# Kernel tuning notes

Hardware: AMD Instinct MI355X
Metric: run time of the kernel (lower is better)

The kernel has to match this reference:

```python
import jax, jax.numpy as jnp
import numpy as np

UNITS = 512
M = 8
INPUT_DIM = 512
BATCH = 2048


def setup_inputs() -> dict:
    key = jax.random.key(0)
    ks = jax.random.split(key, 9)
    D, U = INPUT_DIM, UNITS
    fused_dim = D + U
    def glorot(k, shape):
        lim = np.sqrt(6.0 / (shape[0] + shape[1])).astype(np.float32)
        return jax.random.uniform(k, shape, jnp.float32, -lim, lim)
    return {
        "inputs": jax.random.normal(ks[0], (BATCH, D), jnp.float32),
        "elapsed": jax.random.uniform(ks[1], (BATCH, 1), jnp.float32),
        "state": jax.random.normal(ks[2], (BATCH, U * M), jnp.float32),
        "W_r": glorot(ks[3], (fused_dim, U * M)),
        "b_r": jnp.zeros((U * M,), jnp.float32),
        "W_d": glorot(ks[4], (fused_dim, U)),
        "b_d": jnp.zeros((U,), jnp.float32),
        "W_u": glorot(ks[5], (fused_dim, U * M)),
        "b_u": jnp.zeros((U * M,), jnp.float32),
    }


def reference(inputs, elapsed, state, W_r, b_r, W_d, b_d, W_u, b_u):
    B = inputs.shape[0]
    # tau_i = 10**(i/2)  =>  ln_tau_i = i * 0.5 * ln(10)
    ln_tau_table = 0.5 * jnp.log(jnp.float32(10.0)) * jnp.arange(M, dtype=jnp.float32)  # [M]
    tau_table = jnp.exp(ln_tau_table)  # [M]

    h_hat = state.reshape(B, UNITS, M)            # [B, U, M]
    h = h_hat.sum(axis=2)                          # [B, U]
    fused = jnp.concatenate([inputs, h], axis=-1)  # [B, D+U]

    # retrieval gate: softmax over M buckets of -(ln_tau_r - table)^2
    ln_tau_r = (fused @ W_r + b_r).reshape(B, UNITS, M)
    rki = jax.nn.softmax(-jnp.square(ln_tau_r - ln_tau_table), axis=2)
    q_input = jnp.sum(rki * h_hat, axis=2)         # [B, U]

    # detect (candidate) with tanh
    reset_value = jnp.concatenate([inputs, q_input], axis=1)
    qk = jnp.tanh(reset_value @ W_d + b_d)[:, :, None]  # [B, U, 1]

    # update gate
    ln_tau_s = (fused @ W_u + b_u).reshape(B, UNITS, M)
    ski = jax.nn.softmax(-jnp.square(ln_tau_s - ln_tau_table), axis=2)

    # exponential decay per bucket: elapsed [B,1] / tau [M] -> [B, M]
    exp_term = jnp.exp(-elapsed / tau_table)[:, None, :]  # [B, 1, M]
    h_hat_next = ((1.0 - ski) * h_hat + ski * qk) * exp_term  # [B, U, M]

    h_next = h_hat_next.sum(axis=2)                # [B, U]
    return h_next, h_hat_next.reshape(B, UNITS * M)
```

## Files before the change

kernel.cpp:

```cpp
#include <hip/hip_runtime.h>
#include <hip/hip_fp16.h>
#include <cmath>

#define B_SZ 2048
#define D_IN 512
#define U_N  512
#define FD   1024
#define NRU  4096
#define NRU2 8192

typedef _Float16 f16x8 __attribute__((ext_vector_type(8)));
typedef float    f32x4 __attribute__((ext_vector_type(4)));

typedef const __attribute__((address_space(1))) void glb_cv;
typedef __attribute__((address_space(3))) void lds_v;

#define TAB_INIT {0.0f, 1.15129254649702f, 2.30258509299405f, \
                  3.45387763949107f, 4.60517018598809f, 5.75646273248511f, \
                  6.90775527898214f, 8.05904782547916f}

__global__ __launch_bounds__(256) void prep_kernel(
    const float* __restrict__ inputs, const float* __restrict__ state,
    __half* __restrict__ fused, __half* __restrict__ reset)
{
    const int b = blockIdx.x;
    const int t = threadIdx.x;

    const float2 iv = *(const float2*)(inputs + (size_t)b * D_IN + t * 2);
    __half2 hv;
    hv.x = __float2half(iv.x);
    hv.y = __float2half(iv.y);
    *(__half2*)(fused + (size_t)b * FD + t * 2) = hv;
    *(__half2*)(reset + (size_t)b * FD + t * 2) = hv;

    const float4* sp = (const float4*)(state + (size_t)b * NRU + t * 16);
    float4 x0 = sp[0], x1 = sp[1], x2 = sp[2], x3 = sp[3];
    float s0 = (x0.x + x0.y) + (x0.z + x0.w) + (x1.x + x1.y) + (x1.z + x1.w);
    float s1 = (x2.x + x2.y) + (x2.z + x2.w) + (x3.x + x3.y) + (x3.z + x3.w);
    __half2 h2;
    h2.x = __float2half(s0);
    h2.y = __float2half(s1);
    *(__half2*)(fused + (size_t)b * FD + D_IN + t * 2) = h2;
}

__global__ __launch_bounds__(256) void convT3_kernel(
    const float* __restrict__ W_r, const float* __restrict__ W_u,
    const float* __restrict__ W_d, __half* __restrict__ WruT,
    __half* __restrict__ WdT)
{
    __shared__ float tile[32][33];
    const int bx = blockIdx.x;
    const float* W;
    __half* Wt;
    int N, nt;
    if (bx < 128)      { W = W_r; Wt = WruT;                    N = NRU; nt = bx * 32; }
    else if (bx < 256) { W = W_u; Wt = WruT + (size_t)NRU * FD; N = NRU; nt = (bx - 128) * 32; }
    else               { W = W_d; Wt = WdT;                     N = U_N; nt = (bx - 256) * 32; }

    const int kt = blockIdx.y * 32;
    const int t  = threadIdx.x;
    const int c  = t & 31;
    const int r4 = t >> 5;

#pragma unroll
    for (int i = 0; i < 4; i++) {
        int r = r4 + i * 8;
        tile[r][c] = W[(size_t)(kt + r) * N + nt + c];
    }
    __syncthreads();
#pragma unroll
    for (int i = 0; i < 4; i++) {
        int rr = r4 + i * 8;
        Wt[(size_t)(nt + rr) * FD + kt + c] = __float2half(tile[c][rr]);
    }
}

__global__ __launch_bounds__(512, 2) void gemm_big(
    const __half* __restrict__ A, const __half* __restrict__ Bt,
    const float* __restrict__ b_r, const float* __restrict__ b_u,
    const float* __restrict__ state, __half* __restrict__ resetw,
    __half* __restrict__ skibuf)
{
    __shared__ __align__(16) char smem[131072];
    __half* SAh = (__half*)smem;

    const int t    = threadIdx.x;
    const int m0   = blockIdx.y << 8;
    const int n0   = blockIdx.x << 8;
    const int lane = t & 63;
    const int w    = t >> 6;
    const int wm16 = ((w >> 2) & 1) << 4;
    const int wn16 = (w & 3) << 4;
    const int m16  = lane & 15;
    const int quad = lane >> 4;
    const int g0   = (quad ^ (m16 & 7)) << 3;
    const int g1   = ((quad + 4) ^ (m16 & 7)) << 3;
    const int t8   = t << 3;
    const int trow = t >> 3;
    const int gcol = ((t & 7) ^ (trow & 7)) << 3;

    const __half* gA = A  + (size_t)(m0 + trow) * FD + gcol;
    const __half* gB = Bt + (size_t)(n0 + trow) * FD + gcol;

    f32x4 acc[8][4];
#pragma unroll
    for (int a1 = 0; a1 < 8; a1++)
#pragma unroll
        for (int a2 = 0; a2 < 4; a2++)
            acc[a1][a2] = (f32x4){0.f, 0.f, 0.f, 0.f};

#define BARRIER() __builtin_amdgcn_s_barrier()
#define PRIO1 __builtin_amdgcn_s_setprio(1)
#define PRIO0 __builtin_amdgcn_s_setprio(0)
#define WAITV(n) do { asm volatile("s_waitcnt vmcnt(" #n ")" ::: "memory"); \
                      __builtin_amdgcn_sched_barrier(0); } while (0)
#define WAITL() do { asm volatile("s_waitcnt lgkmcnt(0)" ::: "memory"); \
                     __builtin_amdgcn_sched_barrier(0); } while (0)

#define STAGE_A(buf, h, tt) do { \
        const __half* _s = gA + (size_t)((h) * 128) * FD + (tt) * 64; \
        __half* _d = SAh + (buf) * 32768 + (h) * 8192 + t8; \
        __builtin_amdgcn_global_load_lds((glb_cv*)_s, (lds_v*)_d, 16, 0, 0); \
        __builtin_amdgcn_global_load_lds((glb_cv*)(_s + (size_t)64 * FD), \
                                         (lds_v*)(_d + 4096), 16, 0, 0); } while (0)
#define STAGE_B(buf, h, tt) do { \
        const __half* _s = gB + (size_t)((h) * 128) * FD + (tt) * 64; \
        __half* _d = SAh + (buf) * 32768 + 16384 + (h) * 8192 + t8; \
        __builtin_amdgcn_global_load_lds((glb_cv*)_s, (lds_v*)_d, 16, 0, 0); \
        __builtin_amdgcn_global_load_lds((glb_cv*)(_s + (size_t)64 * FD), \
                                         (lds_v*)(_d + 4096), 16, 0, 0); } while (0)

#define READ_A(c, mh) do { _Pragma("unroll") \
    for (int mi2 = 0; mi2 < 4; mi2++) { \
        const __half* _ap = SAh + (c) * 32768 + \
            ((((mh) * 4 + mi2) * 32 + wm16 + m16) << 6); \
        af[mi2][0] = *(const f16x8*)(_ap + g0); \
        af[mi2][1] = *(const f16x8*)(_ap + g1); } } while (0)
#define READ_B_ALL(c) do { _Pragma("unroll") \
    for (int ni2 = 0; ni2 < 4; ni2++) { \
        const __half* _bp = SAh + (c) * 32768 + 16384 + \
            ((ni2 * 64 + wn16 + m16) << 6); \
        bf[ni2][0] = *(const f16x8*)(_bp + g0); \
        bf[ni2][1] = *(const f16x8*)(_bp + g1); } } while (0)

#define MFMA_Q(MH) do { _Pragma("unroll") \
    for (int ks = 0; ks < 2; ks++) { _Pragma("unroll") \
        for (int mi2 = 0; mi2 < 4; mi2++) { _Pragma("unroll") \
            for (int ni2 = 0; ni2 < 4; ni2++) { \
                acc[(MH)*4+mi2][ni2] = __builtin_amdgcn_mfma_f32_16x16x32_f16( \
                    af[mi2][ks], bf[ni2][ks], acc[(MH)*4+mi2][ni2], 0, 0, 0); } } } } while (0)

    STAGE_B(0, 0, 0); STAGE_B(0, 1, 0);
    STAGE_A(0, 0, 0); STAGE_A(0, 1, 0);
    STAGE_B(1, 0, 1); STAGE_B(1, 1, 1);
    WAITV(4);
    BARRIER();

#pragma unroll 1
    for (int i = 0; i < 8; i++) {
        const int t1 = (2 * i + 1) & 15, t2 = (2 * i + 2) & 15, t3 = (2 * i + 3) & 15;
        f16x8 af[4][2], bf[4][2];
        READ_B_ALL(0); READ_A(0, 0);
        STAGE_A(1, 0, t1); STAGE_A(1, 1, t1);
        WAITL(); PRIO1; MFMA_Q(0); PRIO0; BARRIER();
        READ_A(0, 1);
        STAGE_B(0, 0, t2); STAGE_B(0, 1, t2);
        WAITL(); PRIO1; MFMA_Q(1); PRIO0; WAITV(4); BARRIER();
        READ_B_ALL(1); READ_A(1, 0);
        STAGE_A(0, 0, t2); STAGE_A(0, 1, t2);
        WAITL(); PRIO1; MFMA_Q(0); PRIO0; BARRIER();
        READ_A(1, 1);
        STAGE_B(1, 0, t3); STAGE_B(1, 1, t3);
        WAITL(); PRIO1; MFMA_Q(1); PRIO0; WAITV(4); BARRIER();
    }

    WAITV(0);
    __syncthreads();

#undef BARRIER
#undef PRIO1
#undef PRIO0
#undef WAITV
#undef WAITL
#undef STAGE_A
#undef STAGE_B
#undef READ_A
#undef READ_B_ALL
#undef MFMA_Q

    float*  ebuf = (float*)smem;
    __half* qbuf = (__half*)(smem + 256 * 68 * 4);
    const bool is_r = (n0 < NRU);
    const float* bp = is_r ? b_r : b_u;
    const int n0r = is_r ? n0 : n0 - NRU;
    const float TAB[8] = TAB_INIT;

    for (int ni = 0; ni < 4; ni++) {
        const float bv = bp[n0r + ni * 64 + wn16 + m16];
#pragma unroll
        for (int mi = 0; mi < 8; mi++)
#pragma unroll
            for (int r = 0; r < 4; r++)
                ebuf[(mi * 32 + wm16 + quad * 4 + r) * 68 + wn16 + m16] =
                    acc[mi][ni][r] + bv;
        __syncthreads();

#pragma unroll
        for (int p = 0; p < 4; p++) {
            const int item = p * 512 + t;
            const int row = item >> 3, g = item & 7;
            const int b = m0 + row;
            const float* rp = ebuf + row * 68 + g * 8;
            float v[8];
            *(float4*)&v[0] = *(const float4*)rp;
            *(float4*)&v[4] = *(const float4*)(rp + 4);

            float e[8], sum = 0.f;
#pragma unroll
            for (int i2 = 0; i2 < 8; i2++) {
                float d = v[i2] - TAB[i2];
                e[i2] = __expf(-d * d);
                sum += e[i2];
            }
            const int colr = n0r + ni * 64 + g * 8;
            if (is_r) {
                const float4 h0 = *(const float4*)(state + (size_t)b * NRU + colr);
                const float4 h1 = *(const float4*)(state + (size_t)b * NRU + colr + 4);
                const float hv[8] = {h0.x, h0.y, h0.z, h0.w, h1.x, h1.y, h1.z, h1.w};
                float qn = 0.f;
#pragma unroll
                for (int i2 = 0; i2 < 8; i2++) qn += e[i2] * hv[i2];
                qbuf[row * 8 + g] = __float2half(qn / sum);
            } else {
                const float inv = 1.0f / sum;
                __half2 o[4];
#pragma unroll
                for (int i2 = 0; i2 < 4; i2++) {
                    o[i2].x = __float2half(e[2 * i2] * inv);
                    o[i2].y = __float2half(e[2 * i2 + 1] * inv);
                }
                *(uint4*)(skibuf + (size_t)b * NRU + colr) = *(uint4*)o;
            }
        }
        __syncthreads();
        if (is_r) {
            const int row = t >> 1, lg = (t & 1) << 2;
            uint2 qv = *(uint2*)(qbuf + row * 8 + lg);
            *(uint2*)(resetw + (size_t)(m0 + row) * FD + D_IN + (n0r >> 3) + ni * 8 + lg) = qv;
        }
    }
}

template <int BM, int EPI>
__global__ __launch_bounds__(256) void gemm_k(
    const __half* __restrict__ A, const __half* __restrict__ Bt,
    const float* __restrict__ biasA, const float* __restrict__ biasB, int nsplit,
    float* __restrict__ C, int Ncols,
    const float* __restrict__ state, __half* __restrict__ resetw,
    __half* __restrict__ skibuf, int K)
{
    extern __shared__ __align__(16) char smem[];
    __half* sA = (__half*)smem;
    __half* sB = (__half*)(smem + BM * 128);

    const int t    = threadIdx.x;
    const int m0   = blockIdx.y * BM;
    const int n0   = blockIdx.x << 7;
    const int lane = t & 63;
    const int w    = t >> 6;
    const int m16  = lane & 15;
    const int quad = lane >> 4;
    constexpr int MI = BM / 32;
    constexpr int IA = BM / 32;
    const int wm = (w & 1) * (BM / 2);
    const int wn = (w >> 1) << 6;

    f32x4 acc[MI][4];
#pragma unroll
    for (int i = 0; i < MI; i++)
#pragma unroll
        for (int j = 0; j < 4; j++)
#pragma unroll
            for (int r = 0; r < 4; r++) acc[i][j][r] = 0.f;

    const __half* gAp[IA];
    const __half* lAp[IA];
#pragma unroll
    for (int i = 0; i < IA; i++) {
        const int off = w * (BM * 32) + i * 1024 + lane * 16;
        const int row = off >> 7;
        const int g   = ((off & 127) >> 4) ^ (row & 7);
        gAp[i] = A + (size_t)(m0 + row) * K + g * 8;
        lAp[i] = sA + ((w * (BM * 32) + i * 1024) >> 1);
    }
    const __half* gBp[4];
    const __half* lBp[4];
#pragma unroll
    for (int i = 0; i < 4; i++) {
        const int off = w * 4096 + i * 1024 + lane * 16;
        const int row = off >> 7;
        const int g   = ((off & 127) >> 4) ^ (row & 7);
        gBp[i] = Bt + (size_t)(n0 + row) * K + g * 8;
        lBp[i] = sB + ((w * 4096 + i * 1024) >> 1);
    }

    for (int kt = 0; kt < K; kt += 64) {
        __syncthreads();
#pragma unroll
        for (int i = 0; i < IA; i++)
            __builtin_amdgcn_global_load_lds((glb_cv*)(gAp[i] + kt), (lds_v*)lAp[i], 16, 0, 0);
#pragma unroll
        for (int i = 0; i < 4; i++)
            __builtin_amdgcn_global_load_lds((glb_cv*)(gBp[i] + kt), (lds_v*)lBp[i], 16, 0, 0);
        __syncthreads();

#pragma unroll
        for (int s = 0; s < 2; s++) {
            f16x8 af[MI], bf[4];
#pragma unroll
            for (int mi = 0; mi < MI; mi++) {
                const int row = wm + mi * 16 + m16;
                const int gi  = (s * 4 + quad) ^ (row & 7);
                af[mi] = *(const f16x8*)(sA + row * 64 + gi * 8);
            }
#pragma unroll
            for (int ni = 0; ni < 4; ni++) {
                const int row = wn + ni * 16 + m16;
                const int gi  = (s * 4 + quad) ^ (row & 7);
                bf[ni] = *(const f16x8*)(sB + row * 64 + gi * 8);
            }
#pragma unroll
            for (int mi = 0; mi < MI; mi++)
#pragma unroll
                for (int ni = 0; ni < 4; ni++)
                    acc[mi][ni] = __builtin_amdgcn_mfma_f32_16x16x32_f16(
                        af[mi], bf[ni], acc[mi][ni], 0, 0, 0);
        }
    }

    if constexpr (EPI == 0) {
#pragma unroll
        for (int mi = 0; mi < MI; mi++) {
#pragma unroll
            for (int ni = 0; ni < 4; ni++) {
                const int col = n0 + wn + ni * 16 + m16;
                const float bv = biasA[col];
#pragma unroll
                for (int r = 0; r < 4; r++) {
                    const int row = m0 + wm + mi * 16 + quad * 4 + r;
                    C[(size_t)row * Ncols + col] = tanhf(acc[mi][ni][r] + bv);
                }
            }
        }
    }
}

__global__ __launch_bounds__(256) void final_kernel(
    const __half* __restrict__ skibuf, const float* __restrict__ state,
    const float* __restrict__ qk, const float* __restrict__ elapsed,
    float* __restrict__ out0, float* __restrict__ out1)
{
    const int idx = blockIdx.x * 256 + threadIdx.x;
    const int b = idx >> 9;
    const int u = idx & 511;

    const float INV_TAU[8] = {1.0f, 0.316227766016838f, 0.1f, 0.0316227766016838f,
                              0.01f, 0.00316227766016838f, 0.001f, 0.000316227766016838f};

    const uint4 sr = *(const uint4*)(skibuf + (size_t)b * NRU + u * 8);
    const __half2* sh = (const __half2*)&sr;
    float sk[8];
#pragma unroll
    for (int i = 0; i < 4; i++) {
        float2 f2 = __half22float2(sh[i]);
        sk[2 * i]     = f2.x;
        sk[2 * i + 1] = f2.y;
    }

    const float4* hh = (const float4*)(state + ((size_t)b * NRU + u * 8));
    float4 h0 = hh[0], h1 = hh[1];
    float h[8] = {h0.x, h0.y, h0.z, h0.w, h1.x, h1.y, h1.z, h1.w};

    const float q  = qk[(size_t)b * U_N + u];
    const float el = elapsed[b];

    float hn[8];
    float acc = 0.f;
#pragma unroll
    for (int i = 0; i < 8; i++) {
        const float et = __expf(-el * INV_TAU[i]);
        hn[i] = ((1.0f - sk[i]) * h[i] + sk[i] * q) * et;
        acc += hn[i];
    }

    float4* o = (float4*)(out1 + ((size_t)b * NRU + u * 8));
    o[0] = make_float4(hn[0], hn[1], hn[2], hn[3]);
    o[1] = make_float4(hn[4], hn[5], hn[6], hn[7]);
    out0[(size_t)b * U_N + u] = acc;
}

extern "C" void kernel_launch(void* const* d_in, const int* in_sizes, int n_in,
                              void* d_out, int out_size, void* d_ws, size_t ws_size,
                              hipStream_t stream)
{
    (void)in_sizes; (void)n_in; (void)out_size; (void)ws_size;

    const float* inputs  = (const float*)d_in[0];
    const float* elapsed = (const float*)d_in[1];
    const float* state   = (const float*)d_in[2];
    const float* W_r     = (const float*)d_in[3];
    const float* b_r     = (const float*)d_in[4];
    const float* W_d     = (const float*)d_in[5];
    const float* b_d     = (const float*)d_in[6];
    const float* W_u     = (const float*)d_in[7];
    const float* b_u     = (const float*)d_in[8];
    float* out = (float*)d_out;

    char* ws = (char*)d_ws;
    __half* fused  = (__half*)(ws);
    __half* reset  = (__half*)(ws + ((size_t)4  << 20));
    __half* WruT   = (__half*)(ws + ((size_t)8  << 20));
    __half* WdT    = (__half*)(ws + ((size_t)24 << 20));
    __half* skibuf = (__half*)(ws + ((size_t)25 << 20));
    float*  qk     = (float*) (ws + ((size_t)41 << 20));

    prep_kernel<<<B_SZ, 256, 0, stream>>>(inputs, state, fused, reset);
    convT3_kernel<<<dim3(272, FD / 32), 256, 0, stream>>>(W_r, W_u, W_d, WruT, WdT);

    gemm_big<<<dim3(NRU2 / 256, B_SZ / 256), 512, 0, stream>>>(
        fused, WruT, b_r, b_u, state, reset, skibuf);

    gemm_k<64, 0><<<dim3(U_N / 128, B_SZ / 64), 256, 24576, stream>>>(
        reset, WdT, b_d, nullptr, 1 << 30, qk, U_N, nullptr, nullptr, nullptr, FD);

    final_kernel<<<(B_SZ * U_N) / 256, 256, 0, stream>>>(skibuf, state, qk, elapsed, out,
                                                         out + (size_t)B_SZ * U_N);
}
```

Measured before the change: 202.4 us.

## Use 1024-thread blocks in big GEMM with smaller per-wave tiles

```diff
diff --git a/kernel.cpp b/kernel.cpp
--- a/kernel.cpp
+++ b/kernel.cpp
@@ -75,7 +75,7 @@
     }
 }
 
-__global__ __launch_bounds__(512, 2) void gemm_big(
+__global__ __launch_bounds__(1024, 4) void gemm_big(
     const __half* __restrict__ A, const __half* __restrict__ Bt,
     const float* __restrict__ b_r, const float* __restrict__ b_u,
     const float* __restrict__ state, __half* __restrict__ resetw,
@@ -89,8 +89,8 @@
     const int n0   = blockIdx.x << 8;
     const int lane = t & 63;
     const int w    = t >> 6;
-    const int wm16 = ((w >> 2) & 1) << 4;
-    const int wn16 = (w & 3) << 4;
+    const int wn   = w & 3;
+    const int wm   = w >> 2;
     const int m16  = lane & 15;
     const int quad = lane >> 4;
     const int g0   = (quad ^ (m16 & 7)) << 3;
@@ -102,9 +102,9 @@
     const __half* gA = A  + (size_t)(m0 + trow) * FD + gcol;
     const __half* gB = Bt + (size_t)(n0 + trow) * FD + gcol;
 
-    f32x4 acc[8][4];
-#pragma unroll
-    for (int a1 = 0; a1 < 8; a1++)
+    f32x4 acc[4][4];
+#pragma unroll
+    for (int a1 = 0; a1 < 4; a1++)
 #pragma unroll
         for (int a2 = 0; a2 < 4; a2++)
             acc[a1][a2] = (f32x4){0.f, 0.f, 0.f, 0.f};
@@ -120,58 +120,66 @@
 #define STAGE_A(buf, h, tt) do { \
         const __half* _s = gA + (size_t)((h) * 128) * FD + (tt) * 64; \
         __half* _d = SAh + (buf) * 32768 + (h) * 8192 + t8; \
-        __builtin_amdgcn_global_load_lds((glb_cv*)_s, (lds_v*)_d, 16, 0, 0); \
-        __builtin_amdgcn_global_load_lds((glb_cv*)(_s + (size_t)64 * FD), \
-                                         (lds_v*)(_d + 4096), 16, 0, 0); } while (0)
+        __builtin_amdgcn_global_load_lds((glb_cv*)_s, (lds_v*)_d, 16, 0, 0); } while (0)
 #define STAGE_B(buf, h, tt) do { \
         const __half* _s = gB + (size_t)((h) * 128) * FD + (tt) * 64; \
         __half* _d = SAh + (buf) * 32768 + 16384 + (h) * 8192 + t8; \
-        __builtin_amdgcn_global_load_lds((glb_cv*)_s, (lds_v*)_d, 16, 0, 0); \
-        __builtin_amdgcn_global_load_lds((glb_cv*)(_s + (size_t)64 * FD), \
-                                         (lds_v*)(_d + 4096), 16, 0, 0); } while (0)
+        __builtin_amdgcn_global_load_lds((glb_cv*)_s, (lds_v*)_d, 16, 0, 0); } while (0)
 
 #define READ_A(c, mh) do { _Pragma("unroll") \
-    for (int mi2 = 0; mi2 < 4; mi2++) { \
+    for (int mi2 = 0; mi2 < 2; mi2++) { \
         const __half* _ap = SAh + (c) * 32768 + \
-            ((((mh) * 4 + mi2) * 32 + wm16 + m16) << 6); \
+            (((((mh) * 2 + mi2) * 64) + wm * 16 + m16) << 6); \
         af[mi2][0] = *(const f16x8*)(_ap + g0); \
         af[mi2][1] = *(const f16x8*)(_ap + g1); } } while (0)
 #define READ_B_ALL(c) do { _Pragma("unroll") \
     for (int ni2 = 0; ni2 < 4; ni2++) { \
         const __half* _bp = SAh + (c) * 32768 + 16384 + \
-            ((ni2 * 64 + wn16 + m16) << 6); \
+            ((wn * 64 + ni2 * 16 + m16) << 6); \
         bf[ni2][0] = *(const f16x8*)(_bp + g0); \
         bf[ni2][1] = *(const f16x8*)(_bp + g1); } } while (0)
 
 #define MFMA_Q(MH) do { _Pragma("unroll") \
     for (int ks = 0; ks < 2; ks++) { _Pragma("unroll") \
-        for (int mi2 = 0; mi2 < 4; mi2++) { _Pragma("unroll") \
+        for (int mi2 = 0; mi2 < 2; mi2++) { _Pragma("unroll") \
             for (int ni2 = 0; ni2 < 4; ni2++) { \
-                acc[(MH)*4+mi2][ni2] = __builtin_amdgcn_mfma_f32_16x16x32_f16( \
-                    af[mi2][ks], bf[ni2][ks], acc[(MH)*4+mi2][ni2], 0, 0, 0); } } } } while (0)
+                acc[(MH)*2+mi2][ni2] = __builtin_amdgcn_mfma_f32_16x16x32_f16( \
+                    af[mi2][ks], bf[ni2][ks], acc[(MH)*2+mi2][ni2], 0, 0, 0); } } } } while (0)
 
     STAGE_B(0, 0, 0); STAGE_B(0, 1, 0);
     STAGE_A(0, 0, 0); STAGE_A(0, 1, 0);
     STAGE_B(1, 0, 1); STAGE_B(1, 1, 1);
-    WAITV(4);
+    WAITV(2);
     BARRIER();
 
 #pragma unroll 1
     for (int i = 0; i < 8; i++) {
         const int t1 = (2 * i + 1) & 15, t2 = (2 * i + 2) & 15, t3 = (2 * i + 3) & 15;
-        f16x8 af[4][2], bf[4][2];
-        READ_B_ALL(0); READ_A(0, 0);
-        STAGE_A(1, 0, t1); STAGE_A(1, 1, t1);
-        WAITL(); PRIO1; MFMA_Q(0); PRIO0; BARRIER();
-        READ_A(0, 1);
-        STAGE_B(0, 0, t2); STAGE_B(0, 1, t2);
-        WAITL(); PRIO1; MFMA_Q(1); PRIO0; WAITV(4); BARRIER();
-        READ_B_ALL(1); READ_A(1, 0);
-        STAGE_A(0, 0, t2); STAGE_A(0, 1, t2);
-        WAITL(); PRIO1; MFMA_Q(0); PRIO0; BARRIER();
-        READ_A(1, 1);
-        STAGE_B(1, 0, t3); STAGE_B(1, 1, t3);
-        WAITL(); PRIO1; MFMA_Q(1); PRIO0; WAITV(4); BARRIER();
+        f16x8 bf[4][2];
+        {
+            f16x8 af[2][2];
+            READ_B_ALL(0); READ_A(0, 0);
+            STAGE_A(1, 0, t1); STAGE_A(1, 1, t1);
+            WAITL(); PRIO1; MFMA_Q(0); PRIO0; BARRIER();
+        }
+        {
+            f16x8 af[2][2];
+            READ_A(0, 1);
+            STAGE_B(0, 0, t2); STAGE_B(0, 1, t2);
+            WAITL(); PRIO1; MFMA_Q(1); PRIO0; WAITV(2); BARRIER();
+        }
+        {
+            f16x8 af[2][2];
+            READ_B_ALL(1); READ_A(1, 0);
+            STAGE_A(0, 0, t2); STAGE_A(0, 1, t2);
+            WAITL(); PRIO1; MFMA_Q(0); PRIO0; BARRIER();
+        }
+        {
+            f16x8 af[2][2];
+            READ_A(1, 1);
+            STAGE_B(1, 0, t3); STAGE_B(1, 1, t3);
+            WAITL(); PRIO1; MFMA_Q(1); PRIO0; WAITV(2); BARRIER();
+        }
     }
 
     WAITV(0);
@@ -196,18 +204,18 @@
     const float TAB[8] = TAB_INIT;
 
     for (int ni = 0; ni < 4; ni++) {
-        const float bv = bp[n0r + ni * 64 + wn16 + m16];
-#pragma unroll
-        for (int mi = 0; mi < 8; mi++)
+        const float bv = bp[n0r + wn * 64 + ni * 16 + m16];
+#pragma unroll
+        for (int mi = 0; mi < 4; mi++)
 #pragma unroll
             for (int r = 0; r < 4; r++)
-                ebuf[(mi * 32 + wm16 + quad * 4 + r) * 68 + wn16 + m16] =
+                ebuf[(mi * 64 + wm * 16 + quad * 4 + r) * 68 + wn * 16 + m16] =
                     acc[mi][ni][r] + bv;
         __syncthreads();
 
 #pragma unroll
-        for (int p = 0; p < 4; p++) {
-            const int item = p * 512 + t;
+        for (int p = 0; p < 2; p++) {
+            const int item = p * 1024 + t;
             const int row = item >> 3, g = item & 7;
             const int b = m0 + row;
             const float* rp = ebuf + row * 68 + g * 8;
@@ -222,7 +230,7 @@
                 e[i2] = __expf(-d * d);
                 sum += e[i2];
             }
-            const int colr = n0r + ni * 64 + g * 8;
+            const int colr = n0r + (g >> 1) * 64 + ni * 16 + (g & 1) * 8;
             if (is_r) {
                 const float4 h0 = *(const float4*)(state + (size_t)b * NRU + colr);
                 const float4 h1 = *(const float4*)(state + (size_t)b * NRU + colr + 4);
@@ -244,9 +252,10 @@
         }
         __syncthreads();
         if (is_r) {
-            const int row = t >> 1, lg = (t & 1) << 2;
-            uint2 qv = *(uint2*)(qbuf + row * 8 + lg);
-            *(uint2*)(resetw + (size_t)(m0 + row) * FD + D_IN + (n0r >> 3) + ni * 8 + lg) = qv;
+            const int row = t >> 2, gg = t & 3;
+            const unsigned qv = *(const unsigned*)(qbuf + row * 8 + gg * 2);
+            *(unsigned*)(resetw + (size_t)(m0 + row) * FD + D_IN + (n0r >> 3) +
+                         gg * 8 + ni * 2) = qv;
         }
     }
 }
@@ -427,7 +436,7 @@
     prep_kernel<<<B_SZ, 256, 0, stream>>>(inputs, state, fused, reset);
     convT3_kernel<<<dim3(272, FD / 32), 256, 0, stream>>>(W_r, W_u, W_d, WruT, WdT);
 
-    gemm_big<<<dim3(NRU2 / 256, B_SZ / 256), 512, 0, stream>>>(
+    gemm_big<<<dim3(NRU2 / 256, B_SZ / 256), 1024, 0, stream>>>(
         fused, WruT, b_r, b_u, state, reset, skibuf);
 
     gemm_k<64, 0><<<dim3(U_N / 128, B_SZ / 64), 256, 24576, stream>>>(
```

New measurement: 232.6 us. +15.0%, slower.
